# Performance work log

Hardware: AMD Instinct MI355X
Metric: run time of the kernel (lower is better)

The kernel has to match this reference:

```python
import jax, jax.numpy as jnp
import numpy as np

B, N, C_IN, F, OUT = 32, 1000, 128, 128, 64
RATIOS = (0.8, 0.8)


def setup_inputs() -> dict:
    key = jax.random.key(0)
    ks = jax.random.split(key, 10)
    N_nodes = jax.random.randint(ks[0], (B,), 500, N + 1, dtype=jnp.int32)
    ar = jnp.arange(N)
    mask = (ar[None, :] < N_nodes[:, None]).astype(jnp.float32)  # [B,N]
    A = (jax.random.uniform(ks[1], (B, N, N)) < 0.02).astype(jnp.float32)
    A = A * (1.0 - jnp.eye(N, dtype=jnp.float32))
    A = jnp.maximum(A, A.transpose(0, 2, 1))  # symmetric, no self loops
    A = A * mask[:, :, None] * mask[:, None, :]
    x = jax.random.normal(ks[2], (B, N, C_IN)) * mask[..., None]

    def lin(k, fin, fout):
        bnd = 1.0 / np.sqrt(fin)
        kw, kb = jax.random.split(k)
        W = jax.random.uniform(kw, (fout, fin), minval=-bnd, maxval=bnd)
        b = jax.random.uniform(kb, (fout,), minval=-bnd, maxval=bnd)
        return W, b

    W0, b0 = lin(ks[3], C_IN, F)
    W1, b1 = lin(ks[4], F, F)
    W2, b2 = lin(ks[5], F, F)
    bnd = 1.0 / np.sqrt(F)
    p0 = jax.random.uniform(ks[6], (F, 1), minval=-bnd, maxval=bnd)
    p1 = jax.random.uniform(ks[7], (F, 1), minval=-bnd, maxval=bnd)
    Wfc, bfc = lin(ks[8], F, OUT)
    return dict(x=x, A=A, mask=mask, N_nodes=N_nodes,
                W0=W0, b0=b0, W1=W1, b1=b1, W2=W2, b2=b2,
                p0=p0, p1=p1, Wfc=Wfc, bfc=bfc)


def _gconv(x, A, mask, W, b):
    # K=1 Kipf-Welling conv: L = D^-1/2 (A+I) D^-1/2; relu(Linear(L x)) * mask
    n = A.shape[1]
    A_hat = A + jnp.eye(n, dtype=A.dtype)
    D = (jnp.sum(A_hat, axis=1) + 1e-5) ** -0.5  # [B,N]
    L = D[:, :, None] * A_hat * D[:, None, :]
    h = jnp.einsum('bij,bjc->bic', L, x)
    h = h @ W.T + b
    return jax.nn.relu(h) * mask[..., None]


def _pool(x, A, mask, N_nodes, p, ratio):
    # score each node, drop the N_remove lowest-scoring valid nodes per graph
    y = (x @ p)[..., 0] / jnp.sqrt(jnp.sum(p ** 2))  # [B,N]
    N_remove = (N_nodes.astype(jnp.float32) * (1.0 - ratio)).astype(jnp.int32)
    y_key = jnp.where(mask > 0, y, jnp.inf)  # invalid nodes rank last
    ranks = jnp.argsort(jnp.argsort(y_key, axis=1), axis=1)  # ascending rank
    new_mask = ((ranks >= N_remove[:, None]) & (mask > 0)).astype(x.dtype)
    x = x * jnp.tanh(y)[..., None] * new_mask[..., None]
    A = new_mask[:, :, None] * A * new_mask[:, None, :]
    return x, A, new_mask, N_nodes - N_remove


def reference(x, A, mask, N_nodes, W0, b0, W1, b1, W2, b2, p0, p1, Wfc, bfc):
    h = _gconv(x, A, mask, W0, b0)
    h, A1, m1, n1 = _pool(h, A, mask, N_nodes, p0, RATIOS[0])
    h = _gconv(h, A1, m1, W1, b1)
    h, A2, m2, n2 = _pool(h, A1, m1, n1, p1, RATIOS[1])
    h = _gconv(h, A2, m2, W2, b2)
    g = jnp.max(h, axis=1)  # [B,F] global max pool
    return g @ Wfc.T + bfc  # [B,OUT]
```

## Files before the change

### kernel.cpp

```cpp
#include <hip/hip_runtime.h>
#include <math.h>

#define BB 32
#define NN 1000
#define CC 128
#define FF 128
#define OO 64
#define CAP 128
#define NB 40

#define RMC ((float)(1.0 - 0.8))


__global__ void k_xpin(const float* __restrict__ x, float* __restrict__ xp){
  int blk = blockIdx.x;
  int r = blk & 7, t = blk >> 3;
  int b = r + 8*(t/125), seg = t % 125;
  size_t base = ((size_t)b*NN + seg*8)*CC;
  const float4* src = (const float4*)(x + base);
  float4* dst = (float4*)(xp + base);
  dst[threadIdx.x] = src[threadIdx.x];
}

__global__ void k_csr(const float* __restrict__ A, const float* __restrict__ mask,
                      const int* __restrict__ Nn,
                      const float* __restrict__ p0, const float* __restrict__ p1,
                      const float* __restrict__ W0, const float* __restrict__ W1,
                      const float* __restrict__ W2,
                      short* __restrict__ idx, int* __restrict__ cnt,
                      float* __restrict__ D, float* __restrict__ dg,
                      float* __restrict__ m, float* __restrict__ gate,
                      int* __restrict__ ncur0, float* __restrict__ pn,
                      float* __restrict__ Wt){
  int blk = blockIdx.x, lane = threadIdx.x;
  int r8 = blk & 7, t = blk >> 3;
  int b = r8 + 8*(t/1001), i = t % 1001;
  if (i == NN){
    for (int j = lane; j < NN; j += 64){
      float v = mask[b*NN + j]; m[b*NN + j] = v; gate[b*NN + j] = v;
    }
    if (lane == 0) ncur0[b] = Nn[b];
    if (b == 0 && lane == 1){ float s=0.f; for(int c=0;c<FF;c++) s += p0[c]*p0[c]; pn[0] = sqrtf(s); }
    if (b == 1 && lane == 1){ float s=0.f; for(int c=0;c<FF;c++) s += p1[c]*p1[c]; pn[1] = sqrtf(s); }
    for (int e = b*1536 + lane; e < (b+1)*1536; e += 64){
      int s = e / (FF*CC), rem = e % (FF*CC);
      int c = rem >> 7, f = rem & 127;
      const float* W = (s == 0) ? W0 : (s == 1) ? W1 : W2;
      Wt[(size_t)s*FF*CC + rem] = W[f*CC + c];
    }
    return;
  }
  if (mask[b*NN + i] == 0.f){
    if (lane == 0){
      cnt[b*NN + i] = 0;
      D[b*NN + i]  = 1.0f / sqrtf(1.0f + 1e-5f);
      dg[b*NN + i] = 0.f;
    }
    return;
  }
  const float4* row = (const float4*)(A + ((size_t)b*NN + i)*NN);
  short* out = idx + ((size_t)b*NN + i)*CAP;
  int count = 0;
  for (int base = 0; base < 250; base += 64){
    int q = base + lane;
    float4 v;
    if (q < 250) v = row[q]; else { v.x=v.y=v.z=v.w=0.f; }
    int lc = (v.x!=0.f) + (v.y!=0.f) + (v.z!=0.f) + (v.w!=0.f);
    int pre = lc;
    #pragma unroll
    for (int off = 1; off < 64; off <<= 1){
      int t2 = __shfl_up(pre, off);
      if (lane >= off) pre += t2;
    }
    int tot = __shfl(pre, 63);
    pre -= lc;
    int slot = count + pre;
    int j = q*4;
    if (v.x!=0.f && slot < CAP) out[slot++] = (short)j;
    if (v.y!=0.f && slot < CAP) out[slot++] = (short)(j+1);
    if (v.z!=0.f && slot < CAP) out[slot++] = (short)(j+2);
    if (v.w!=0.f && slot < CAP) out[slot++] = (short)(j+3);
    count += tot;
  }
  if (lane == 0){
    int cn = (count < CAP) ? count : CAP;
    cnt[b*NN + i] = cn;
    float Dv = 1.0f / sqrtf((float)cn + 1.0f + 1e-5f);
    D[b*NN + i]  = Dv;
    dg[b*NN + i] = Dv;
  }
}

__global__ void k_aggt(const short* __restrict__ idx, const int* __restrict__ cnt,
                       const float* __restrict__ D, const float* __restrict__ dg,
                       const float* __restrict__ m, const float* __restrict__ gate,
                       const float* __restrict__ h, float* __restrict__ T){
  __shared__ int   nb[4][CAP];
  __shared__ float dn[4][CAP];
  int blk = blockIdx.x;
  int b   = (blk & 7) + 8*((blk >> 3) & 3);
  int rem = blk >> 5;
  int tid = threadIdx.x;
  int w = tid >> 6, lane = tid & 63;
  int i = rem*4 + w;
  int g = lane >> 5, l32 = lane & 31;
  size_t orow = ((size_t)b*NN + i)*CC;
  const float* hb = h + (size_t)b*NN*CC;
  if (m[b*NN + i] == 0.f){
    if (g == 0){ float4 z = {0.f,0.f,0.f,0.f}; *(float4*)(T + orow + (l32<<2)) = z; }
    return;
  }
  int n = cnt[b*NN + i];
  const short* r = idx + ((size_t)b*NN + i)*CAP;
  int*   nbw = nb[w];
  float* dnw = dn[w];
  int j0 = 0; float d0 = 0.f; bool k0 = false;
  if (lane < n){ j0 = (int)r[lane]; d0 = dg[b*NN + j0]; k0 = (d0 != 0.f); }
  unsigned long long bal = __ballot(k0);
  int pre = __popcll(bal & ((1ull << lane) - 1ull));
  if (k0){ nbw[pre] = j0*CC; dnw[pre] = d0; }
  int nlive = __popcll(bal);
  if (n > 64){
    int e = lane + 64; int j1 = 0; float d1 = 0.f; bool k1 = false;
    if (e < n){ j1 = (int)r[e]; d1 = dg[b*NN + j1]; k1 = (d1 != 0.f); }
    unsigned long long bal1 = __ballot(k1);
    int pre1 = __popcll(bal1 & ((1ull << lane) - 1ull));
    if (k1){ nbw[nlive + pre1] = j1*CC; dnw[nlive + pre1] = d1; }
    nlive += __popcll(bal1);
  }
  int np = (nlive + 15) & ~15;
  if (lane < np - nlive){ nbw[nlive + lane] = 0; dnw[nlive + lane] = 0.f; }
  __builtin_amdgcn_wave_barrier();
  float4 a0 = {0.f,0.f,0.f,0.f}, a1 = a0, a2 = a0, a3 = a0;
  for (int k = 0; k < np; k += 16){
    int e = k + g;
    float4 v0 = *(const float4*)(hb + nbw[e   ] + (l32<<2));
    float4 v1 = *(const float4*)(hb + nbw[e+ 2] + (l32<<2));
    float4 v2 = *(const float4*)(hb + nbw[e+ 4] + (l32<<2));
    float4 v3 = *(const float4*)(hb + nbw[e+ 6] + (l32<<2));
    float4 v4 = *(const float4*)(hb + nbw[e+ 8] + (l32<<2));
    float4 v5 = *(const float4*)(hb + nbw[e+10] + (l32<<2));
    float4 v6 = *(const float4*)(hb + nbw[e+12] + (l32<<2));
    float4 v7 = *(const float4*)(hb + nbw[e+14] + (l32<<2));
    float e0 = dnw[e], e1 = dnw[e+2], e2 = dnw[e+4], e3 = dnw[e+6];
    float e4 = dnw[e+8], e5 = dnw[e+10], e6 = dnw[e+12], e7 = dnw[e+14];
    a0.x += e0*v0.x; a0.y += e0*v0.y; a0.z += e0*v0.z; a0.w += e0*v0.w;
    a1.x += e1*v1.x; a1.y += e1*v1.y; a1.z += e1*v1.z; a1.w += e1*v1.w;
    a2.x += e2*v2.x; a2.y += e2*v2.y; a2.z += e2*v2.z; a2.w += e2*v2.w;
    a3.x += e3*v3.x; a3.y += e3*v3.y; a3.z += e3*v3.z; a3.w += e3*v3.w;
    a0.x += e4*v4.x; a0.y += e4*v4.y; a0.z += e4*v4.z; a0.w += e4*v4.w;
    a1.x += e5*v5.x; a1.y += e5*v5.y; a1.z += e5*v5.z; a1.w += e5*v5.w;
    a2.x += e6*v6.x; a2.y += e6*v6.y; a2.z += e6*v6.z; a2.w += e6*v6.w;
    a3.x += e7*v7.x; a3.y += e7*v7.y; a3.z += e7*v7.z; a3.w += e7*v7.w;
  }
  float4 Y;
  Y.x = (a0.x + a1.x) + (a2.x + a3.x);
  Y.y = (a0.y + a1.y) + (a2.y + a3.y);
  Y.z = (a0.z + a1.z) + (a2.z + a3.z);
  Y.w = (a0.w + a1.w) + (a2.w + a3.w);
  Y.x += __shfl_xor(Y.x, 32);
  Y.y += __shfl_xor(Y.y, 32);
  Y.z += __shfl_xor(Y.z, 32);
  Y.w += __shfl_xor(Y.w, 32);
  float Di = D[b*NN + i];
  float gi = gate[b*NN + i];
  if (g == 0){
    float4 hv = *(const float4*)(hb + (size_t)i*CC + (l32<<2));
    float4 o;
    o.x = Di*Y.x + Di*Di*(gi*hv.x);
    o.y = Di*Y.y + Di*Di*(gi*hv.y);
    o.z = Di*Y.z + Di*Di*(gi*hv.z);
    o.w = Di*Y.w + Di*Di*(gi*hv.w);
    *(float4*)(T + orow + (l32<<2)) = o;
  }
}

__global__ void k_lin(const float* __restrict__ T, const float* __restrict__ m,
                      const float* __restrict__ Wt,
                      const float* __restrict__ bias, float* __restrict__ Hout){
  __shared__ float t[NB][CC];
  int blk = blockIdx.x, tid = threadIdx.x;
  int r8 = blk & 7, tq = blk >> 3;
  int b = r8 + 8*(tq/25);
  int i0 = (tq % 25) * NB;
  const float4* Tg = (const float4*)(T + ((size_t)b*NN + i0)*CC);
  float4* tl = (float4*)&t[0][0];
  #pragma unroll
  for (int e = 0; e < 5; e++) tl[tid + e*256] = Tg[tid + e*256];
  __syncthreads();
  int fg = tid & 31;
  int nr = tid >> 5;
  float acc[5][4];
  float4 bi = ((const float4*)bias)[fg];
  #pragma unroll
  for (int n5 = 0; n5 < 5; n5++){
    acc[n5][0]=bi.x; acc[n5][1]=bi.y; acc[n5][2]=bi.z; acc[n5][3]=bi.w;
  }
  for (int c4 = 0; c4 < 32; c4++){
    float4 tv[5];
    #pragma unroll
    for (int n5 = 0; n5 < 5; n5++)
      tv[n5] = *((const float4*)&t[nr + n5*8][c4*4]);
    #pragma unroll
    for (int k = 0; k < 4; k++){
      float4 wv = ((const float4*)Wt)[(size_t)(c4*4 + k)*32 + fg];
      #pragma unroll
      for (int n5 = 0; n5 < 5; n5++){
        float tvv = (k==0) ? tv[n5].x : (k==1) ? tv[n5].y : (k==2) ? tv[n5].z : tv[n5].w;
        acc[n5][0] += tvv*wv.x; acc[n5][1] += tvv*wv.y;
        acc[n5][2] += tvv*wv.z; acc[n5][3] += tvv*wv.w;
      }
    }
  }
  #pragma unroll
  for (int n5 = 0; n5 < 5; n5++){
    int i = i0 + nr + n5*8;
    float mi = m[b*NN + i];
    float4 o4;
    o4.x = fmaxf(acc[n5][0], 0.f)*mi;
    o4.y = fmaxf(acc[n5][1], 0.f)*mi;
    o4.z = fmaxf(acc[n5][2], 0.f)*mi;
    o4.w = fmaxf(acc[n5][3], 0.f)*mi;
    ((float4*)&Hout[((size_t)b*NN + i)*CC])[fg] = o4;
  }
}

__global__ void k_score(const float* __restrict__ H, const float* __restrict__ p,
                        const float* __restrict__ pn, float* __restrict__ y){
  int blk = blockIdx.x, lane = threadIdx.x;
  int r8 = blk & 7, t = blk >> 3;
  int b = r8 + 8*(t/1000), i = t % 1000;
  const float* hrow = H + ((size_t)b*NN + i)*CC;
  float s = hrow[lane]*p[lane] + hrow[lane+64]*p[lane+64];
  for (int off = 32; off > 0; off >>= 1) s += __shfl_down(s, off);
  if (lane == 0) y[b*NN + i] = s / pn[0];
}

__global__ void k_pool(const float* __restrict__ y, float* __restrict__ m,
                       const int* __restrict__ ncur_in, int* __restrict__ ncur_out,
                       float* __restrict__ gate){
  __shared__ float yk[NN];
  int blk = blockIdx.x, tid = threadIdx.x;
  int r8 = blk & 7, t = blk >> 3;
  int b = r8 + 8*(t >> 2), xx = t & 3;
  int i = xx*256 + tid;
  for (int j = tid; j < NN; j += 256)
    yk[j] = (m[b*NN + j] > 0.f) ? y[b*NN + j] : INFINITY;
  __syncthreads();
  int n = ncur_in[b];
  int nr = (int)((float)n * RMC);
  float myv = (i < NN) ? yk[i] : INFINITY;
  int cnt = 0;
  const float4* yk4 = (const float4*)yk;
  #pragma unroll 5
  for (int q = 0; q < 250; q++){
    float4 v = yk4[q];
    int j0 = q*4;
    cnt += (int)((v.x < myv) || (v.x == myv && j0     < i));
    cnt += (int)((v.y < myv) || (v.y == myv && j0 + 1 < i));
    cnt += (int)((v.z < myv) || (v.z == myv && j0 + 2 < i));
    cnt += (int)((v.w < myv) || (v.w == myv && j0 + 3 < i));
  }
  if (i < NN){
    bool keep = (cnt >= nr) && (m[b*NN + i] > 0.f);
    m[b*NN + i]    = keep ? 1.0f : 0.0f;
    gate[b*NN + i] = keep ? tanhf(y[b*NN + i]) : 0.0f;
  }
  if (xx == 0 && tid == 0) ncur_out[b] = n - nr;
}

__global__ void k_deg(const short* __restrict__ idx, const int* __restrict__ cnt,
                      const float* __restrict__ m, const float* __restrict__ gate,
                      float* __restrict__ D, float* __restrict__ dg){
  __shared__ float ml[NN];
  int blk = blockIdx.x, tid = threadIdx.x;
  int r8 = blk & 7, t = blk >> 3;
  int b = r8 + 8*(t >> 2), xx = t & 3;
  for (int i = tid; i < NN; i += 256) ml[i] = m[b*NN + i];
  __syncthreads();
  int j = xx*250 + tid;
  if (tid < 250){
    const short* r = idx + ((size_t)b*NN + j)*CAP;
    int n = cnt[b*NN + j];
    float s0=0.f, s1=0.f, s2=0.f, s3=0.f;
    int k = 0;
    for (; k+4 <= n; k += 4){
      s0 += ml[r[k]]; s1 += ml[r[k+1]]; s2 += ml[r[k+2]]; s3 += ml[r[k+3]];
    }
    for (; k < n; k++) s0 += ml[r[k]];
    float Dv = 1.0f / sqrtf(((s0+s1)+(s2+s3)) + 1.0f + 1e-5f);
    D[b*NN + j]  = Dv;
    dg[b*NN + j] = Dv * gate[b*NN + j];
  }
}

__global__ void k_fmax(const float* __restrict__ H, const float* __restrict__ m,
                       float* __restrict__ part){
  int blk = blockIdx.x, c = threadIdx.x;
  int r8 = blk & 7, t = blk >> 3;
  int b = r8 + 8*(t >> 3), sx = t & 7;
  float mx = 0.f;
  int i0 = sx*125;
  for (int i = i0; i < i0+125; i++){
    if (m[b*NN + i] != 0.f)
      mx = fmaxf(mx, H[((size_t)b*NN + i)*CC + c]);
  }
  part[((size_t)b*8 + sx)*CC + c] = mx;
}

__global__ void k_fc(const float* __restrict__ part, const float* __restrict__ Wfc,
                     const float* __restrict__ bfc, float* __restrict__ out){
  __shared__ float g[FF];
  int b = blockIdx.x, tid = threadIdx.x;
  float mx = 0.f;
  #pragma unroll
  for (int s = 0; s < 8; s++) mx = fmaxf(mx, part[((size_t)b*8 + s)*CC + tid]);
  g[tid] = mx;
  __syncthreads();
  if (tid < OO){
    float acc = bfc[tid];
    for (int c = 0; c < FF; c++) acc += g[c]*Wfc[tid*FF + c];
    out[b*OO + tid] = acc;
  }
}

extern "C" void kernel_launch(void* const* d_in, const int* in_sizes, int n_in,
                              void* d_out, int out_size, void* d_ws, size_t ws_size,
                              hipStream_t stream) {
  const float* x    = (const float*)d_in[0];
  const float* A    = (const float*)d_in[1];
  const float* mask = (const float*)d_in[2];
  const int*   Nn   = (const int*)  d_in[3];
  const float* W0   = (const float*)d_in[4];
  const float* b0   = (const float*)d_in[5];
  const float* W1   = (const float*)d_in[6];
  const float* b1   = (const float*)d_in[7];
  const float* W2   = (const float*)d_in[8];
  const float* b2   = (const float*)d_in[9];
  const float* p0   = (const float*)d_in[10];
  const float* p1   = (const float*)d_in[11];
  const float* Wfc  = (const float*)d_in[12];
  const float* bfc  = (const float*)d_in[13];
  float* out = (float*)d_out;

  char* w = (char*)d_ws;
  float* H   = (float*)w; w += (size_t)BB*NN*CC*4;
  float* T   = (float*)w; w += (size_t)BB*NN*CC*4;
  short* idx = (short*)w; w += (size_t)BB*NN*CAP*2;
  float* Wt  = (float*)w; w += (size_t)3*FF*CC*4;
  float* part= (float*)w; w += (size_t)8*BB*CC*4;
  int*   cnt = (int*)w;   w += (size_t)BB*NN*4;
  float* D   = (float*)w; w += (size_t)BB*NN*4;
  float* m   = (float*)w; w += (size_t)BB*NN*4;
  float* ysc = (float*)w; w += (size_t)BB*NN*4;
  float* gate= (float*)w; w += (size_t)BB*NN*4;
  float* dg  = (float*)w; w += (size_t)BB*NN*4;
  int*   ncur= (int*)w;   w += 3*BB*sizeof(int);
  float* pn  = (float*)w; w += 64;
  float* xp  = (float*)w; w += (size_t)BB*NN*CC*4;

  k_xpin<<<4000, 256, 0, stream>>>(x, xp);
  k_csr<<<32032, 64, 0, stream>>>(A, mask, Nn, p0, p1, W0, W1, W2,
                                  idx, cnt, D, dg, m, gate, ncur, pn, Wt);

  k_aggt<<<(BB*NN)/4, 256, 0, stream>>>(idx, cnt, D, dg, m, gate, xp, T);
  k_lin<<<800, 256, 0, stream>>>(T, m, Wt + 0*FF*CC, b0, H);
  k_score<<<32000, 64, 0, stream>>>(H, p0, pn + 0, ysc);
  k_pool<<<128, 256, 0, stream>>>(ysc, m, ncur + 0*BB, ncur + 1*BB, gate);
  k_deg<<<128, 256, 0, stream>>>(idx, cnt, m, gate, D, dg);

  k_aggt<<<(BB*NN)/4, 256, 0, stream>>>(idx, cnt, D, dg, m, gate, H, T);
  k_lin<<<800, 256, 0, stream>>>(T, m, Wt + 1*FF*CC, b1, H);
  k_score<<<32000, 64, 0, stream>>>(H, p1, pn + 1, ysc);
  k_pool<<<128, 256, 0, stream>>>(ysc, m, ncur + 1*BB, ncur + 2*BB, gate);
  k_deg<<<128, 256, 0, stream>>>(idx, cnt, m, gate, D, dg);

  k_aggt<<<(BB*NN)/4, 256, 0, stream>>>(idx, cnt, D, dg, m, gate, H, T);
  k_lin<<<800, 256, 0, stream>>>(T, m, Wt + 2*FF*CC, b2, H);

  k_fmax<<<256, 128, 0, stream>>>(H, m, part);
  k_fc<<<BB, 128, 0, stream>>>(part, Wfc, bfc, out);
}
```

Measured before the change: 449.9 us.

## Fuse neighbor aggregation into linear kernel and drop input copy

Merges the sparse aggregation kernel into the linear-layer kernel: each 40-row block computes the aggregated rows directly into shared memory, then applies the weight matrix, so the intermediate T buffer is never written to or re-read from global memory. It also removes the x-to-workspace copy kernel and reads x directly, and ping-pongs between two H buffers because input and output can no longer alias. The trade-off is fewer blocks (800 instead of 8000), each looping over 10 row groups sequentially, which lowers parallelism and latency hiding for the gather phase.

After: 446.8 us. Within noise of the previous version (-0.7%).

```diff
diff --git a/kernel.cpp b/kernel.cpp
--- a/kernel.cpp
+++ b/kernel.cpp
@@ -11,16 +11,6 @@
 
 #define RMC ((float)(1.0 - 0.8))
 
-
-__global__ void k_xpin(const float* __restrict__ x, float* __restrict__ xp){
-  int blk = blockIdx.x;
-  int r = blk & 7, t = blk >> 3;
-  int b = r + 8*(t/125), seg = t % 125;
-  size_t base = ((size_t)b*NN + seg*8)*CC;
-  const float4* src = (const float4*)(x + base);
-  float4* dst = (float4*)(xp + base);
-  dst[threadIdx.x] = src[threadIdx.x];
-}
 
 __global__ void k_csr(const float* __restrict__ A, const float* __restrict__ mask,
                       const int* __restrict__ Nn,
@@ -91,102 +81,93 @@
   }
 }
 
-__global__ void k_aggt(const short* __restrict__ idx, const int* __restrict__ cnt,
-                       const float* __restrict__ D, const float* __restrict__ dg,
-                       const float* __restrict__ m, const float* __restrict__ gate,
-                       const float* __restrict__ h, float* __restrict__ T){
+__global__ void k_agglin(const short* __restrict__ idx, const int* __restrict__ cnt,
+                         const float* __restrict__ D, const float* __restrict__ dg,
+                         const float* __restrict__ m, const float* __restrict__ gate,
+                         const float* __restrict__ h,
+                         const float* __restrict__ Wt,
+                         const float* __restrict__ bias, float* __restrict__ Hout){
+  __shared__ float t[NB][CC];
   __shared__ int   nb[4][CAP];
   __shared__ float dn[4][CAP];
-  int blk = blockIdx.x;
-  int b   = (blk & 7) + 8*((blk >> 3) & 3);
-  int rem = blk >> 5;
-  int tid = threadIdx.x;
-  int w = tid >> 6, lane = tid & 63;
-  int i = rem*4 + w;
-  int g = lane >> 5, l32 = lane & 31;
-  size_t orow = ((size_t)b*NN + i)*CC;
-  const float* hb = h + (size_t)b*NN*CC;
-  if (m[b*NN + i] == 0.f){
-    if (g == 0){ float4 z = {0.f,0.f,0.f,0.f}; *(float4*)(T + orow + (l32<<2)) = z; }
-    return;
-  }
-  int n = cnt[b*NN + i];
-  const short* r = idx + ((size_t)b*NN + i)*CAP;
-  int*   nbw = nb[w];
-  float* dnw = dn[w];
-  int j0 = 0; float d0 = 0.f; bool k0 = false;
-  if (lane < n){ j0 = (int)r[lane]; d0 = dg[b*NN + j0]; k0 = (d0 != 0.f); }
-  unsigned long long bal = __ballot(k0);
-  int pre = __popcll(bal & ((1ull << lane) - 1ull));
-  if (k0){ nbw[pre] = j0*CC; dnw[pre] = d0; }
-  int nlive = __popcll(bal);
-  if (n > 64){
-    int e = lane + 64; int j1 = 0; float d1 = 0.f; bool k1 = false;
-    if (e < n){ j1 = (int)r[e]; d1 = dg[b*NN + j1]; k1 = (d1 != 0.f); }
-    unsigned long long bal1 = __ballot(k1);
-    int pre1 = __popcll(bal1 & ((1ull << lane) - 1ull));
-    if (k1){ nbw[nlive + pre1] = j1*CC; dnw[nlive + pre1] = d1; }
-    nlive += __popcll(bal1);
-  }
-  int np = (nlive + 15) & ~15;
-  if (lane < np - nlive){ nbw[nlive + lane] = 0; dnw[nlive + lane] = 0.f; }
-  __builtin_amdgcn_wave_barrier();
-  float4 a0 = {0.f,0.f,0.f,0.f}, a1 = a0, a2 = a0, a3 = a0;
-  for (int k = 0; k < np; k += 16){
-    int e = k + g;
-    float4 v0 = *(const float4*)(hb + nbw[e   ] + (l32<<2));
-    float4 v1 = *(const float4*)(hb + nbw[e+ 2] + (l32<<2));
-    float4 v2 = *(const float4*)(hb + nbw[e+ 4] + (l32<<2));
-    float4 v3 = *(const float4*)(hb + nbw[e+ 6] + (l32<<2));
-    float4 v4 = *(const float4*)(hb + nbw[e+ 8] + (l32<<2));
-    float4 v5 = *(const float4*)(hb + nbw[e+10] + (l32<<2));
-    float4 v6 = *(const float4*)(hb + nbw[e+12] + (l32<<2));
-    float4 v7 = *(const float4*)(hb + nbw[e+14] + (l32<<2));
-    float e0 = dnw[e], e1 = dnw[e+2], e2 = dnw[e+4], e3 = dnw[e+6];
-    float e4 = dnw[e+8], e5 = dnw[e+10], e6 = dnw[e+12], e7 = dnw[e+14];
-    a0.x += e0*v0.x; a0.y += e0*v0.y; a0.z += e0*v0.z; a0.w += e0*v0.w;
-    a1.x += e1*v1.x; a1.y += e1*v1.y; a1.z += e1*v1.z; a1.w += e1*v1.w;
-    a2.x += e2*v2.x; a2.y += e2*v2.y; a2.z += e2*v2.z; a2.w += e2*v2.w;
-    a3.x += e3*v3.x; a3.y += e3*v3.y; a3.z += e3*v3.z; a3.w += e3*v3.w;
-    a0.x += e4*v4.x; a0.y += e4*v4.y; a0.z += e4*v4.z; a0.w += e4*v4.w;
-    a1.x += e5*v5.x; a1.y += e5*v5.y; a1.z += e5*v5.z; a1.w += e5*v5.w;
-    a2.x += e6*v6.x; a2.y += e6*v6.y; a2.z += e6*v6.z; a2.w += e6*v6.w;
-    a3.x += e7*v7.x; a3.y += e7*v7.y; a3.z += e7*v7.z; a3.w += e7*v7.w;
-  }
-  float4 Y;
-  Y.x = (a0.x + a1.x) + (a2.x + a3.x);
-  Y.y = (a0.y + a1.y) + (a2.y + a3.y);
-  Y.z = (a0.z + a1.z) + (a2.z + a3.z);
-  Y.w = (a0.w + a1.w) + (a2.w + a3.w);
-  Y.x += __shfl_xor(Y.x, 32);
-  Y.y += __shfl_xor(Y.y, 32);
-  Y.z += __shfl_xor(Y.z, 32);
-  Y.w += __shfl_xor(Y.w, 32);
-  float Di = D[b*NN + i];
-  float gi = gate[b*NN + i];
-  if (g == 0){
-    float4 hv = *(const float4*)(hb + (size_t)i*CC + (l32<<2));
-    float4 o;
-    o.x = Di*Y.x + Di*Di*(gi*hv.x);
-    o.y = Di*Y.y + Di*Di*(gi*hv.y);
-    o.z = Di*Y.z + Di*Di*(gi*hv.z);
-    o.w = Di*Y.w + Di*Di*(gi*hv.w);
-    *(float4*)(T + orow + (l32<<2)) = o;
-  }
-}
-
-__global__ void k_lin(const float* __restrict__ T, const float* __restrict__ m,
-                      const float* __restrict__ Wt,
-                      const float* __restrict__ bias, float* __restrict__ Hout){
-  __shared__ float t[NB][CC];
   int blk = blockIdx.x, tid = threadIdx.x;
   int r8 = blk & 7, tq = blk >> 3;
   int b = r8 + 8*(tq/25);
   int i0 = (tq % 25) * NB;
-  const float4* Tg = (const float4*)(T + ((size_t)b*NN + i0)*CC);
-  float4* tl = (float4*)&t[0][0];
-  #pragma unroll
-  for (int e = 0; e < 5; e++) tl[tid + e*256] = Tg[tid + e*256];
+  int w = tid >> 6, lane = tid & 63;
+  int g = lane >> 5, l32 = lane & 31;
+  const float* hb = h + (size_t)b*NN*CC;
+  int*   nbw = nb[w];
+  float* dnw = dn[w];
+  for (int q = 0; q < 10; q++){
+    int lr = q*4 + w;
+    int i  = i0 + lr;
+    if (m[b*NN + i] == 0.f){
+      if (g == 0){ float4 z = {0.f,0.f,0.f,0.f}; *(float4*)&t[lr][l32<<2] = z; }
+      continue;
+    }
+    int n = cnt[b*NN + i];
+    const short* r = idx + ((size_t)b*NN + i)*CAP;
+    int j0 = 0; float d0 = 0.f; bool k0 = false;
+    if (lane < n){ j0 = (int)r[lane]; d0 = dg[b*NN + j0]; k0 = (d0 != 0.f); }
+    unsigned long long bal = __ballot(k0);
+    int pre = __popcll(bal & ((1ull << lane) - 1ull));
+    if (k0){ nbw[pre] = j0*CC; dnw[pre] = d0; }
+    int nlive = __popcll(bal);
+    if (n > 64){
+      int e = lane + 64; int j1 = 0; float d1 = 0.f; bool k1 = false;
+      if (e < n){ j1 = (int)r[e]; d1 = dg[b*NN + j1]; k1 = (d1 != 0.f); }
+      unsigned long long bal1 = __ballot(k1);
+      int pre1 = __popcll(bal1 & ((1ull << lane) - 1ull));
+      if (k1){ nbw[nlive + pre1] = j1*CC; dnw[nlive + pre1] = d1; }
+      nlive += __popcll(bal1);
+    }
+    int np = (nlive + 15) & ~15;
+    if (lane < np - nlive){ nbw[nlive + lane] = 0; dnw[nlive + lane] = 0.f; }
+    __builtin_amdgcn_wave_barrier();
+    float4 a0 = {0.f,0.f,0.f,0.f}, a1 = a0, a2 = a0, a3 = a0;
+    for (int k = 0; k < np; k += 16){
+      int e = k + g;
+      float4 v0 = *(const float4*)(hb + nbw[e   ] + (l32<<2));
+      float4 v1 = *(const float4*)(hb + nbw[e+ 2] + (l32<<2));
+      float4 v2 = *(const float4*)(hb + nbw[e+ 4] + (l32<<2));
+      float4 v3 = *(const float4*)(hb + nbw[e+ 6] + (l32<<2));
+      float4 v4 = *(const float4*)(hb + nbw[e+ 8] + (l32<<2));
+      float4 v5 = *(const float4*)(hb + nbw[e+10] + (l32<<2));
+      float4 v6 = *(const float4*)(hb + nbw[e+12] + (l32<<2));
+      float4 v7 = *(const float4*)(hb + nbw[e+14] + (l32<<2));
+      float e0 = dnw[e], e1 = dnw[e+2], e2 = dnw[e+4], e3 = dnw[e+6];
+      float e4 = dnw[e+8], e5 = dnw[e+10], e6 = dnw[e+12], e7 = dnw[e+14];
+      a0.x += e0*v0.x; a0.y += e0*v0.y; a0.z += e0*v0.z; a0.w += e0*v0.w;
+      a1.x += e1*v1.x; a1.y += e1*v1.y; a1.z += e1*v1.z; a1.w += e1*v1.w;
+      a2.x += e2*v2.x; a2.y += e2*v2.y; a2.z += e2*v2.z; a2.w += e2*v2.w;
+      a3.x += e3*v3.x; a3.y += e3*v3.y; a3.z += e3*v3.z; a3.w += e3*v3.w;
+      a0.x += e4*v4.x; a0.y += e4*v4.y; a0.z += e4*v4.z; a0.w += e4*v4.w;
+      a1.x += e5*v5.x; a1.y += e5*v5.y; a1.z += e5*v5.z; a1.w += e5*v5.w;
+      a2.x += e6*v6.x; a2.y += e6*v6.y; a2.z += e6*v6.z; a2.w += e6*v6.w;
+      a3.x += e7*v7.x; a3.y += e7*v7.y; a3.z += e7*v7.z; a3.w += e7*v7.w;
+    }
+    float4 Y;
+    Y.x = (a0.x + a1.x) + (a2.x + a3.x);
+    Y.y = (a0.y + a1.y) + (a2.y + a3.y);
+    Y.z = (a0.z + a1.z) + (a2.z + a3.z);
+    Y.w = (a0.w + a1.w) + (a2.w + a3.w);
+    Y.x += __shfl_xor(Y.x, 32);
+    Y.y += __shfl_xor(Y.y, 32);
+    Y.z += __shfl_xor(Y.z, 32);
+    Y.w += __shfl_xor(Y.w, 32);
+    float Di = D[b*NN + i];
+    float gi = gate[b*NN + i];
+    if (g == 0){
+      float4 hv = *(const float4*)(hb + (size_t)i*CC + (l32<<2));
+      float4 o;
+      o.x = Di*Y.x + Di*Di*(gi*hv.x);
+      o.y = Di*Y.y + Di*Di*(gi*hv.y);
+      o.z = Di*Y.z + Di*Di*(gi*hv.z);
+      o.w = Di*Y.w + Di*Di*(gi*hv.w);
+      *(float4*)&t[lr][l32<<2] = o;
+    }
+  }
   __syncthreads();
   int fg = tid & 31;
   int nr = tid >> 5;
@@ -345,7 +326,7 @@
 
   char* w = (char*)d_ws;
   float* H   = (float*)w; w += (size_t)BB*NN*CC*4;
-  float* T   = (float*)w; w += (size_t)BB*NN*CC*4;
+  float* H2  = (float*)w; w += (size_t)BB*NN*CC*4;
   short* idx = (short*)w; w += (size_t)BB*NN*CAP*2;
   float* Wt  = (float*)w; w += (size_t)3*FF*CC*4;
   float* part= (float*)w; w += (size_t)8*BB*CC*4;
@@ -357,26 +338,24 @@
   float* dg  = (float*)w; w += (size_t)BB*NN*4;
   int*   ncur= (int*)w;   w += 3*BB*sizeof(int);
   float* pn  = (float*)w; w += 64;
-  float* xp  = (float*)w; w += (size_t)BB*NN*CC*4;
-
-  k_xpin<<<4000, 256, 0, stream>>>(x, xp);
+
   k_csr<<<32032, 64, 0, stream>>>(A, mask, Nn, p0, p1, W0, W1, W2,
                                   idx, cnt, D, dg, m, gate, ncur, pn, Wt);
 
-  k_aggt<<<(BB*NN)/4, 256, 0, stream>>>(idx, cnt, D, dg, m, gate, xp, T);
-  k_lin<<<800, 256, 0, stream>>>(T, m, Wt + 0*FF*CC, b0, H);
+  k_agglin<<<800, 256, 0, stream>>>(idx, cnt, D, dg, m, gate, x,
+                                    Wt + 0*FF*CC, b0, H);
   k_score<<<32000, 64, 0, stream>>>(H, p0, pn + 0, ysc);
   k_pool<<<128, 256, 0, stream>>>(ysc, m, ncur + 0*BB, ncur + 1*BB, gate);
   k_deg<<<128, 256, 0, stream>>>(idx, cnt, m, gate, D, dg);
 
-  k_aggt<<<(BB*NN)/4, 256, 0, stream>>>(idx, cnt, D, dg, m, gate, H, T);
-  k_lin<<<800, 256, 0, stream>>>(T, m, Wt + 1*FF*CC, b1, H);
-  k_score<<<32000, 64, 0, stream>>>(H, p1, pn + 1, ysc);
+  k_agglin<<<800, 256, 0, stream>>>(idx, cnt, D, dg, m, gate, H,
+                                    Wt + 1*FF*CC, b1, H2);
+  k_score<<<32000, 64, 0, stream>>>(H2, p1, pn + 1, ysc);
   k_pool<<<128, 256, 0, stream>>>(ysc, m, ncur + 1*BB, ncur + 2*BB, gate);
   k_deg<<<128, 256, 0, stream>>>(idx, cnt, m, gate, D, dg);
 
-  k_aggt<<<(BB*NN)/4, 256, 0, stream>>>(idx, cnt, D, dg, m, gate, H, T);
-  k_lin<<<800, 256, 0, stream>>>(T, m, Wt + 2*FF*CC, b2, H);
+  k_agglin<<<800, 256, 0, stream>>>(idx, cnt, D, dg, m, gate, H2,
+                                    Wt + 2*FF*CC, b2, H);
 
   k_fmax<<<256, 128, 0, stream>>>(H, m, part);
   k_fc<<<BB, 128, 0, stream>>>(part, Wfc, bfc, out);
```
